# Optimization experiments

Hardware: AMD Instinct MI355X
Metric: run time of the kernel (lower is better)

Reference implementation:

```python
import jax, jax.numpy as jnp
import numpy as np

N = 4_000_000
POINT_DIM = 2
FEAT_OUT = 64
NUM_SEGMENTS = 4096


def setup_inputs() -> dict:
    key = jax.random.key(0)
    k1, k2, k3, k4 = jax.random.split(key, 4)
    x = jax.random.normal(k1, (N, POINT_DIM), dtype=jnp.float32)
    segment_ids = jnp.sort(jax.random.randint(k2, (N,), 0, NUM_SEGMENTS, dtype=jnp.int64 if jax.config.jax_enable_x64 else jnp.int32))
    W = jax.random.normal(k3, (POINT_DIM, FEAT_OUT), dtype=jnp.float32) / np.sqrt(POINT_DIM)
    b = jax.random.normal(k4, (FEAT_OUT,), dtype=jnp.float32)
    return {"x": x, "segment_ids": segment_ids, "W": W, "b": b, "num_segments": NUM_SEGMENTS}


def reference(x, segment_ids, W, b, num_segments):
    # phi: per-point linear projection, [N, point_dim] -> [N, feat_out]
    h = x @ W + b
    # 'add' aggregation over each set == segment sum (ids are sorted per-set)
    out = jax.ops.segment_sum(h, segment_ids, num_segments=num_segments,
                              indices_are_sorted=True)
    return out  # [num_segments, feat_out]
```

## Files before the change

kernel.cpp:

```cpp
#include <hip/hip_runtime.h>
#include <stdint.h>

#define NSEG 4096


__global__ __launch_bounds__(256) void seg_reduce(
    const float4* __restrict__ x4,
    const int4*   __restrict__ ids4,
    float* __restrict__ acc,
    int nchunk)
{
    const int lane = threadIdx.x & 63;
    const int idx = blockIdx.x * blockDim.x + threadIdx.x;
    const bool valid = idx < nchunk;

    int4 id0, id1, id2, id3;
    float4 xv[8];
    if (valid) {
        id0 = ids4[4 * idx + 0];
        id1 = ids4[4 * idx + 1];
        id2 = ids4[4 * idx + 2];
        id3 = ids4[4 * idx + 3];
        #pragma unroll
        for (int i = 0; i < 8; ++i) xv[i] = x4[8 * idx + i];
    } else {
        id0 = make_int4(-1, -1, -1, -1);
        id1 = id0; id2 = id0; id3 = id0;
        #pragma unroll
        for (int i = 0; i < 8; ++i) xv[i] = make_float4(0.f, 0.f, 0.f, 0.f);
    }

    int cur;
    float s0, s1, cnt;

    if (id0.x == id3.w) {
        cur = id0.x;
        float a0 = 0.f, a1 = 0.f;
        #pragma unroll
        for (int i = 0; i < 8; ++i) {
            a0 += xv[i].x + xv[i].z;
            a1 += xv[i].y + xv[i].w;
        }
        s0 = a0; s1 = a1;
        cnt = valid ? 16.f : 0.f;
    } else {
        int segs[16];
        segs[0] = id0.x;  segs[1] = id0.y;  segs[2] = id0.z;  segs[3] = id0.w;
        segs[4] = id1.x;  segs[5] = id1.y;  segs[6] = id1.z;  segs[7] = id1.w;
        segs[8] = id2.x;  segs[9] = id2.y;  segs[10] = id2.z; segs[11] = id2.w;
        segs[12] = id3.x; segs[13] = id3.y; segs[14] = id3.z; segs[15] = id3.w;
        float p0[16], p1[16];
        #pragma unroll
        for (int i = 0; i < 8; ++i) {
            p0[2 * i]     = xv[i].x;  p1[2 * i]     = xv[i].y;
            p0[2 * i + 1] = xv[i].z;  p1[2 * i + 1] = xv[i].w;
        }
        cur = segs[0]; s0 = p0[0]; s1 = p1[0]; cnt = 1.f;
        #pragma unroll
        for (int i = 1; i < 16; ++i) {
            if (segs[i] != cur) {
                atomicAdd(&acc[4 * cur + 0], s0);
                atomicAdd(&acc[4 * cur + 1], s1);
                atomicAdd(&acc[4 * cur + 2], cnt);
                cur = segs[i]; s0 = p0[i]; s1 = p1[i]; cnt = 1.f;
            } else {
                s0 += p0[i]; s1 += p1[i]; cnt += 1.f;
            }
        }
    }

    int prev = __shfl_up(cur, 1);
    bool head = (lane == 0) || (prev != cur);
    uint64_t heads = __ballot(head);
    uint64_t below = heads & (~0ull >> (63 - lane));
    int run_start = 63 - __builtin_clzll(below);

    #pragma unroll
    for (int d = 1; d < 64; d <<= 1) {
        float t0 = __shfl_up(s0, d);
        float t1 = __shfl_up(s1, d);
        float tc = __shfl_up(cnt, d);
        if (lane - d >= run_start) { s0 += t0; s1 += t1; cnt += tc; }
    }

    bool tail = (lane == 63) || ((heads >> (lane + 1)) & 1ull);
    if (tail && cur >= 0) {
        atomicAdd(&acc[4 * cur + 0], s0);
        atomicAdd(&acc[4 * cur + 1], s1);
        atomicAdd(&acc[4 * cur + 2], cnt);
    }
}

__global__ __launch_bounds__(256) void epilogue(
    const float*  __restrict__ acc,
    const float4* __restrict__ W4,
    const float4* __restrict__ b4,
    float4* __restrict__ out4)
{
    int idx = blockIdx.x * blockDim.x + threadIdx.x;
    int s = idx >> 4;
    int f = idx & 15;
    float a0 = acc[4 * s], a1 = acc[4 * s + 1], c = acc[4 * s + 2];
    float4 w0 = W4[f], w1 = W4[16 + f], bb = b4[f];
    float4 o;
    o.x = a0 * w0.x + a1 * w1.x + c * bb.x;
    o.y = a0 * w0.y + a1 * w1.y + c * bb.y;
    o.z = a0 * w0.z + a1 * w1.z + c * bb.z;
    o.w = a0 * w0.w + a1 * w1.w + c * bb.w;
    out4[idx] = o;
}

extern "C" void kernel_launch(void* const* d_in, const int* in_sizes, int n_in,
                              void* d_out, int out_size, void* d_ws, size_t ws_size,
                              hipStream_t stream) {
    const float4* x4   = (const float4*)d_in[0];
    const int4*   ids4 = (const int4*)d_in[1];
    const float4* W4   = (const float4*)d_in[2];
    const float4* b4   = (const float4*)d_in[3];
    float4* out4 = (float4*)d_out;

    const int n = in_sizes[1];
    const int nchunk = n / 16;
    const int nblocks = (nchunk + 255) / 256;

    float* acc = (float*)d_ws;

    hipMemsetAsync(d_ws, 0, 4 * NSEG * sizeof(float), stream);
    seg_reduce<<<nblocks, 256, 0, stream>>>(x4, ids4, acc, nchunk);
    epilogue<<<(NSEG * 64 / 4) / 256, 256, 0, stream>>>(acc, W4, b4, out4);
}
```

Measured before the change: 92.34 us.

## Restructure segment reduce to coalesced per-wave strided loads with per-iteration wave scans

```diff
diff --git a/kernel.cpp b/kernel.cpp
--- a/kernel.cpp
+++ b/kernel.cpp
@@ -3,91 +3,79 @@
 
 #define NSEG 4096
 
-
 __global__ __launch_bounds__(256) void seg_reduce(
     const float4* __restrict__ x4,
     const int4*   __restrict__ ids4,
     float* __restrict__ acc,
-    int nchunk)
+    int n)
 {
     const int lane = threadIdx.x & 63;
-    const int idx = blockIdx.x * blockDim.x + threadIdx.x;
-    const bool valid = idx < nchunk;
+    const int wave = threadIdx.x >> 6;
+    const int wc   = blockIdx.x * 4 + wave;
+    const int base_pt = wc * 1024;
+    if (base_pt >= n) return;
 
-    int4 id0, id1, id2, id3;
-    float4 xv[8];
-    if (valid) {
-        id0 = ids4[4 * idx + 0];
-        id1 = ids4[4 * idx + 1];
-        id2 = ids4[4 * idx + 2];
-        id3 = ids4[4 * idx + 3];
-        #pragma unroll
-        for (int i = 0; i < 8; ++i) xv[i] = x4[8 * idx + i];
-    } else {
-        id0 = make_int4(-1, -1, -1, -1);
-        id1 = id0; id2 = id0; id3 = id0;
-        #pragma unroll
-        for (int i = 0; i < 8; ++i) xv[i] = make_float4(0.f, 0.f, 0.f, 0.f);
-    }
-
-    int cur;
-    float s0, s1, cnt;
-
-    if (id0.x == id3.w) {
-        cur = id0.x;
-        float a0 = 0.f, a1 = 0.f;
-        #pragma unroll
-        for (int i = 0; i < 8; ++i) {
-            a0 += xv[i].x + xv[i].z;
-            a1 += xv[i].y + xv[i].w;
-        }
-        s0 = a0; s1 = a1;
-        cnt = valid ? 16.f : 0.f;
-    } else {
-        int segs[16];
-        segs[0] = id0.x;  segs[1] = id0.y;  segs[2] = id0.z;  segs[3] = id0.w;
-        segs[4] = id1.x;  segs[5] = id1.y;  segs[6] = id1.z;  segs[7] = id1.w;
-        segs[8] = id2.x;  segs[9] = id2.y;  segs[10] = id2.z; segs[11] = id2.w;
-        segs[12] = id3.x; segs[13] = id3.y; segs[14] = id3.z; segs[15] = id3.w;
-        float p0[16], p1[16];
-        #pragma unroll
-        for (int i = 0; i < 8; ++i) {
-            p0[2 * i]     = xv[i].x;  p1[2 * i]     = xv[i].y;
-            p0[2 * i + 1] = xv[i].z;  p1[2 * i + 1] = xv[i].w;
-        }
-        cur = segs[0]; s0 = p0[0]; s1 = p1[0]; cnt = 1.f;
-        #pragma unroll
-        for (int i = 1; i < 16; ++i) {
-            if (segs[i] != cur) {
-                atomicAdd(&acc[4 * cur + 0], s0);
-                atomicAdd(&acc[4 * cur + 1], s1);
-                atomicAdd(&acc[4 * cur + 2], cnt);
-                cur = segs[i]; s0 = p0[i]; s1 = p1[i]; cnt = 1.f;
-            } else {
-                s0 += p0[i]; s1 += p1[i]; cnt += 1.f;
-            }
-        }
-    }
-
-    int prev = __shfl_up(cur, 1);
-    bool head = (lane == 0) || (prev != cur);
-    uint64_t heads = __ballot(head);
-    uint64_t below = heads & (~0ull >> (63 - lane));
-    int run_start = 63 - __builtin_clzll(below);
+    const int m_base = base_pt >> 2;
+    const int k_base = base_pt >> 1;
 
     #pragma unroll
-    for (int d = 1; d < 64; d <<= 1) {
-        float t0 = __shfl_up(s0, d);
-        float t1 = __shfl_up(s1, d);
-        float tc = __shfl_up(cnt, d);
-        if (lane - d >= run_start) { s0 += t0; s1 += t1; cnt += tc; }
-    }
+    for (int j = 0; j < 4; ++j) {
+        const int pt0 = base_pt + 256 * j + 4 * lane;
+        const bool v = pt0 < n;
 
-    bool tail = (lane == 63) || ((heads >> (lane + 1)) & 1ull);
-    if (tail && cur >= 0) {
-        atomicAdd(&acc[4 * cur + 0], s0);
-        atomicAdd(&acc[4 * cur + 1], s1);
-        atomicAdd(&acc[4 * cur + 2], cnt);
+        int4   q;
+        float4 A, B;
+        if (v) {
+            q = ids4[m_base + 64 * j + lane];
+            A = x4[k_base + 128 * j + 2 * lane];
+            B = x4[k_base + 128 * j + 2 * lane + 1];
+        } else {
+            q = make_int4(-1, -1, -1, -1);
+            A = make_float4(0.f, 0.f, 0.f, 0.f);
+            B = A;
+        }
+
+        int cur; float s0, s1, cnt;
+        if (q.x == q.w) {
+            cur = q.x;
+            s0  = A.x + A.z + B.x + B.z;
+            s1  = A.y + A.w + B.y + B.w;
+            cnt = (cur >= 0) ? 4.f : 0.f;
+        } else {
+            cur = q.x; s0 = A.x; s1 = A.y; cnt = 1.f;
+            #define PROC(SEG, X0, X1)                              \
+                if ((SEG) != cur) {                                \
+                    atomicAdd(&acc[4 * cur + 0], s0);              \
+                    atomicAdd(&acc[4 * cur + 1], s1);              \
+                    atomicAdd(&acc[4 * cur + 2], cnt);             \
+                    cur = (SEG); s0 = (X0); s1 = (X1); cnt = 1.f;  \
+                } else { s0 += (X0); s1 += (X1); cnt += 1.f; }
+            PROC(q.y, A.z, A.w)
+            PROC(q.z, B.x, B.y)
+            PROC(q.w, B.z, B.w)
+            #undef PROC
+        }
+
+        int prev = __shfl_up(cur, 1);
+        bool head = (lane == 0) || (prev != cur);
+        uint64_t heads = __ballot(head);
+        uint64_t below = heads & (~0ull >> (63 - lane));
+        int run_start = 63 - __builtin_clzll(below);
+
+        #pragma unroll
+        for (int d = 1; d < 64; d <<= 1) {
+            float t0 = __shfl_up(s0, d);
+            float t1 = __shfl_up(s1, d);
+            float tc = __shfl_up(cnt, d);
+            if (lane - d >= run_start) { s0 += t0; s1 += t1; cnt += tc; }
+        }
+
+        bool tail = (lane == 63) || ((heads >> (lane + 1)) & 1ull);
+        if (tail && cur >= 0) {
+            atomicAdd(&acc[4 * cur + 0], s0);
+            atomicAdd(&acc[4 * cur + 1], s1);
+            atomicAdd(&acc[4 * cur + 2], cnt);
+        }
     }
 }
 
@@ -120,12 +108,12 @@
     float4* out4 = (float4*)d_out;
 
     const int n = in_sizes[1];
-    const int nchunk = n / 16;
-    const int nblocks = (nchunk + 255) / 256;
+    const int nwave_chunks = (n + 1023) / 1024;
+    const int nblocks = (nwave_chunks + 3) / 4;
 
     float* acc = (float*)d_ws;
 
     hipMemsetAsync(d_ws, 0, 4 * NSEG * sizeof(float), stream);
-    seg_reduce<<<nblocks, 256, 0, stream>>>(x4, ids4, acc, nchunk);
+    seg_reduce<<<nblocks, 256, 0, stream>>>(x4, ids4, acc, n);
     epilogue<<<(NSEG * 64 / 4) / 256, 256, 0, stream>>>(acc, W4, b4, out4);
 }
```

Result: no change. 92.28 us (-0.1%).
